# Performance work log

Measured on AMD Instinct MI355X. Metric: run time of the kernel, lower is better.

The kernel has to match this reference:

```python
import jax, jax.numpy as jnp
import numpy as np

N_NODES = 10000
N_EDGES = 320000
D = 128      # node/edge feature dim
H = 512      # MLP hidden width


def _mlp(x, W1, b1, W2, b2):
    return jax.nn.relu(x @ W1 + b1) @ W2 + b2


def setup_inputs() -> dict:
    key = jax.random.key(0)
    ks = jax.random.split(key, 8)
    s = lambda fan_in: 1.0 / np.sqrt(fan_in)
    return {
        "x": jax.random.normal(ks[0], (N_NODES, D), jnp.float32),
        "edge_index": jax.random.randint(ks[1], (2, N_EDGES), 0, N_NODES, jnp.int64),
        "edge_attr": jax.random.normal(ks[2], (N_EDGES, D), jnp.float32),
        "We1": jax.random.normal(ks[3], (3 * D, H), jnp.float32) * s(3 * D),
        "be1": jnp.zeros((H,), jnp.float32),
        "We2": jax.random.normal(ks[4], (H, D), jnp.float32) * s(H),
        "be2": jnp.zeros((D,), jnp.float32),
        "Wn1": jax.random.normal(ks[5], (2 * D, H), jnp.float32) * s(2 * D),
        "bn1": jnp.zeros((H,), jnp.float32),
        "Wn2": jax.random.normal(ks[6], (H, D), jnp.float32) * s(H),
        "bn2": jnp.zeros((D,), jnp.float32),
    }


def reference(x, edge_index, edge_attr, We1, be1, We2, be2, Wn1, bn1, Wn2, bn2):
    senders = edge_index[0]
    receivers = edge_index[1]
    # gather -> edge MLP
    edge_inputs = jnp.concatenate([x[senders], x[receivers], edge_attr], axis=-1)  # [E, 3D]
    updated_edge_attr = _mlp(edge_inputs, We1, be1, We2, be2)                      # [E, D]
    # scatter-add into receiving nodes
    aggregated = jax.ops.segment_sum(updated_edge_attr, receivers, num_segments=x.shape[0])  # [N, D]
    # node MLP
    node_inputs = jnp.concatenate([x, aggregated], axis=-1)                        # [N, 2D]
    updated_nodes = _mlp(node_inputs, Wn1, bn1, Wn2, bn2)                          # [N, D]
    return updated_nodes, updated_edge_attr
```

## Files before the change

### kernel.cpp

```cpp
#include <hip/hip_runtime.h>
#include <hip/hip_bf16.h>

#define N_NODES 10000
#define N_EDGES 320000
#define D 128
#define H 512

typedef __bf16 bf16x8 __attribute__((ext_vector_type(8)));
typedef float f32x4 __attribute__((ext_vector_type(4)));
typedef unsigned short u16x8 __attribute__((ext_vector_type(8)));

__device__ __forceinline__ unsigned short f2bf(float f) {
    union { float f; unsigned u; } v; v.f = f;
    unsigned r = v.u + 0x7fffu + ((v.u >> 16) & 1u);
    return (unsigned short)(r >> 16);
}

__global__ void cast_x_kernel(const float* __restrict__ x, unsigned short* __restrict__ xb) {
    int t = blockIdx.x * 256 + threadIdx.x;
    float4 v = reinterpret_cast<const float4*>(x)[t];
    ushort4 o;
    o.x = f2bf(v.x); o.y = f2bf(v.y); o.z = f2bf(v.z); o.w = f2bf(v.w);
    reinterpret_cast<ushort4*>(xb)[t] = o;
}

__global__ void swizzle_w_kernel(const float* __restrict__ W, unsigned short* __restrict__ out,
                                 int K, int Nn) {
    int t = blockIdx.x * 256 + threadIdx.x;
    int total = (K >> 5) * (Nn >> 4) * 64;
    if (t >= total) return;
    int lane = t & 63;
    int tile = t >> 6;
    int ntiles = Nn >> 4;
    int nt = tile % ntiles;
    int kt = tile / ntiles;
    int k0 = kt * 32 + (lane >> 4) * 8;
    int n  = nt * 16 + (lane & 15);
    unsigned short tmp[8];
#pragma unroll
    for (int j = 0; j < 8; ++j) tmp[j] = f2bf(W[(size_t)(k0 + j) * Nn + n]);
    ushort4* dst = reinterpret_cast<ushort4*>(out + (size_t)t * 8);
    dst[0] = *reinterpret_cast<ushort4*>(&tmp[0]);
    dst[1] = *reinterpret_cast<ushort4*>(&tmp[4]);
}

__global__ __launch_bounds__(256) void edge_mlp_kernel(
    const unsigned short* __restrict__ xb,
    const int* __restrict__ eidx,
    const float* __restrict__ edge_attr,
    const unsigned short* __restrict__ We1s,
    const float* __restrict__ be1,
    const unsigned short* __restrict__ We2s,
    const float* __restrict__ be2,
    float* __restrict__ out_edges,
    float* __restrict__ agg)
{
    __shared__ unsigned short sA[64 * 392];
    __shared__ unsigned short sH[64 * 136];

    const int tid = threadIdx.x;
    const int wave = tid >> 6, lane = tid & 63;
    const int e0 = blockIdx.x * 64;
    const int l15 = lane & 15;
    const int q8 = (lane >> 4) * 8;

#pragma unroll
    for (int seg = 0; seg < 2; ++seg) {
        for (int c = tid; c < 1024; c += 256) {
            int row = c >> 4;
            int off = (c & 15) << 3;
            int e = e0 + row;
            int node = eidx[seg * N_EDGES + e];
            *reinterpret_cast<bf16x8*>(&sA[row * 392 + seg * 128 + off]) =
                *reinterpret_cast<const bf16x8*>(&xb[(size_t)node * 128 + off]);
        }
    }
    for (int c = tid; c < 1024; c += 256) {
        int row = c >> 4;
        int off = (c & 15) << 3;
        int e = e0 + row;
        const float4* src = reinterpret_cast<const float4*>(&edge_attr[(size_t)e * 128 + off]);
        float4 v0 = src[0], v1 = src[1];
        u16x8 o;
        o[0] = f2bf(v0.x); o[1] = f2bf(v0.y); o[2] = f2bf(v0.z); o[3] = f2bf(v0.w);
        o[4] = f2bf(v1.x); o[5] = f2bf(v1.y); o[6] = f2bf(v1.z); o[7] = f2bf(v1.w);
        *reinterpret_cast<u16x8*>(&sA[row * 392 + 256 + off]) = o;
    }
    __syncthreads();

    f32x4 acc2[2][4];
#pragma unroll
    for (int nn = 0; nn < 2; ++nn)
#pragma unroll
        for (int mt = 0; mt < 4; ++mt) acc2[nn][mt] = (f32x4){0.f, 0.f, 0.f, 0.f};

#pragma unroll 1
    for (int h = 0; h < 4; ++h) {
        f32x4 acc1[2][4];
#pragma unroll
        for (int nn = 0; nn < 2; ++nn)
#pragma unroll
            for (int mt = 0; mt < 4; ++mt) acc1[nn][mt] = (f32x4){0.f, 0.f, 0.f, 0.f};

#pragma unroll
        for (int kt = 0; kt < 12; ++kt) {
            bf16x8 a[4];
#pragma unroll
            for (int mt = 0; mt < 4; ++mt)
                a[mt] = *reinterpret_cast<const bf16x8*>(&sA[(mt * 16 + l15) * 392 + kt * 32 + q8]);
#pragma unroll
            for (int nn = 0; nn < 2; ++nn) {
                int ntile = h * 8 + wave * 2 + nn;
                bf16x8 b = *reinterpret_cast<const bf16x8*>(
                    &We1s[(((size_t)kt * 32 + ntile) * 64 + lane) * 8]);
#pragma unroll
                for (int mt = 0; mt < 4; ++mt)
                    acc1[nn][mt] = __builtin_amdgcn_mfma_f32_16x16x32_bf16(a[mt], b, acc1[nn][mt], 0, 0, 0);
            }
        }

        __syncthreads();
#pragma unroll
        for (int nn = 0; nn < 2; ++nn) {
            int cc = (wave * 2 + nn) * 16 + l15;
            float bias = be1[h * 128 + cc];
#pragma unroll
            for (int mt = 0; mt < 4; ++mt)
#pragma unroll
                for (int r = 0; r < 4; ++r) {
                    float v = acc1[nn][mt][r] + bias;
                    v = v > 0.f ? v : 0.f;
                    int row = mt * 16 + (lane >> 4) * 4 + r;
                    sH[row * 136 + cc] = f2bf(v);
                }
        }
        __syncthreads();

#pragma unroll
        for (int kt = 0; kt < 4; ++kt) {
            bf16x8 a[4];
#pragma unroll
            for (int mt = 0; mt < 4; ++mt)
                a[mt] = *reinterpret_cast<const bf16x8*>(&sH[(mt * 16 + l15) * 136 + kt * 32 + q8]);
#pragma unroll
            for (int nn = 0; nn < 2; ++nn) {
                int ntile = wave * 2 + nn;
                bf16x8 b = *reinterpret_cast<const bf16x8*>(
                    &We2s[(((size_t)(h * 4 + kt) * 8 + ntile) * 64 + lane) * 8]);
#pragma unroll
                for (int mt = 0; mt < 4; ++mt)
                    acc2[nn][mt] = __builtin_amdgcn_mfma_f32_16x16x32_bf16(a[mt], b, acc2[nn][mt], 0, 0, 0);
            }
        }
    }

#pragma unroll
    for (int nn = 0; nn < 2; ++nn) {
        int cc = (wave * 2 + nn) * 16 + l15;
        float bias = be2[cc];
#pragma unroll
        for (int mt = 0; mt < 4; ++mt)
#pragma unroll
            for (int r = 0; r < 4; ++r) {
                int row = mt * 16 + (lane >> 4) * 4 + r;
                int e = e0 + row;
                float v = acc2[nn][mt][r] + bias;
                out_edges[(size_t)e * 128 + cc] = v;
                int recv = eidx[N_EDGES + e];
                atomicAdd(&agg[(size_t)recv * 128 + cc], v);
            }
    }
}

__global__ __launch_bounds__(256) void node_mlp_kernel(
    const unsigned short* __restrict__ xb,
    const float* __restrict__ agg,
    const unsigned short* __restrict__ Wn1s,
    const float* __restrict__ bn1,
    const unsigned short* __restrict__ Wn2s,
    const float* __restrict__ bn2,
    float* __restrict__ out_nodes)
{
    __shared__ unsigned short sA[64 * 264];
    __shared__ unsigned short sH[64 * 136];

    const int tid = threadIdx.x;
    const int wave = tid >> 6, lane = tid & 63;
    const int n0 = blockIdx.x * 64;
    const int l15 = lane & 15;
    const int q8 = (lane >> 4) * 8;

    for (int c = tid; c < 1024; c += 256) {
        int row = c >> 4;
        int off = (c & 15) << 3;
        int node = n0 + row;
        bf16x8 v = {};
        if (node < N_NODES)
            v = *reinterpret_cast<const bf16x8*>(&xb[(size_t)node * 128 + off]);
        *reinterpret_cast<bf16x8*>(&sA[row * 264 + off]) = v;
    }
    for (int c = tid; c < 1024; c += 256) {
        int row = c >> 4;
        int off = (c & 15) << 3;
        int node = n0 + row;
        u16x8 o = {0, 0, 0, 0, 0, 0, 0, 0};
        if (node < N_NODES) {
            const float4* src = reinterpret_cast<const float4*>(&agg[(size_t)node * 128 + off]);
            float4 v0 = src[0], v1 = src[1];
            o[0] = f2bf(v0.x); o[1] = f2bf(v0.y); o[2] = f2bf(v0.z); o[3] = f2bf(v0.w);
            o[4] = f2bf(v1.x); o[5] = f2bf(v1.y); o[6] = f2bf(v1.z); o[7] = f2bf(v1.w);
        }
        *reinterpret_cast<u16x8*>(&sA[row * 264 + 128 + off]) = o;
    }
    __syncthreads();

    f32x4 acc2[2][4];
#pragma unroll
    for (int nn = 0; nn < 2; ++nn)
#pragma unroll
        for (int mt = 0; mt < 4; ++mt) acc2[nn][mt] = (f32x4){0.f, 0.f, 0.f, 0.f};

#pragma unroll 1
    for (int h = 0; h < 4; ++h) {
        f32x4 acc1[2][4];
#pragma unroll
        for (int nn = 0; nn < 2; ++nn)
#pragma unroll
            for (int mt = 0; mt < 4; ++mt) acc1[nn][mt] = (f32x4){0.f, 0.f, 0.f, 0.f};

#pragma unroll
        for (int kt = 0; kt < 8; ++kt) {
            bf16x8 a[4];
#pragma unroll
            for (int mt = 0; mt < 4; ++mt)
                a[mt] = *reinterpret_cast<const bf16x8*>(&sA[(mt * 16 + l15) * 264 + kt * 32 + q8]);
#pragma unroll
            for (int nn = 0; nn < 2; ++nn) {
                int ntile = h * 8 + wave * 2 + nn;
                bf16x8 b = *reinterpret_cast<const bf16x8*>(
                    &Wn1s[(((size_t)kt * 32 + ntile) * 64 + lane) * 8]);
#pragma unroll
                for (int mt = 0; mt < 4; ++mt)
                    acc1[nn][mt] = __builtin_amdgcn_mfma_f32_16x16x32_bf16(a[mt], b, acc1[nn][mt], 0, 0, 0);
            }
        }

        __syncthreads();
#pragma unroll
        for (int nn = 0; nn < 2; ++nn) {
            int cc = (wave * 2 + nn) * 16 + l15;
            float bias = bn1[h * 128 + cc];
#pragma unroll
            for (int mt = 0; mt < 4; ++mt)
#pragma unroll
                for (int r = 0; r < 4; ++r) {
                    float v = acc1[nn][mt][r] + bias;
                    v = v > 0.f ? v : 0.f;
                    int row = mt * 16 + (lane >> 4) * 4 + r;
                    sH[row * 136 + cc] = f2bf(v);
                }
        }
        __syncthreads();

#pragma unroll
        for (int kt = 0; kt < 4; ++kt) {
            bf16x8 a[4];
#pragma unroll
            for (int mt = 0; mt < 4; ++mt)
                a[mt] = *reinterpret_cast<const bf16x8*>(&sH[(mt * 16 + l15) * 136 + kt * 32 + q8]);
#pragma unroll
            for (int nn = 0; nn < 2; ++nn) {
                int ntile = wave * 2 + nn;
                bf16x8 b = *reinterpret_cast<const bf16x8*>(
                    &Wn2s[(((size_t)(h * 4 + kt) * 8 + ntile) * 64 + lane) * 8]);
#pragma unroll
                for (int mt = 0; mt < 4; ++mt)
                    acc2[nn][mt] = __builtin_amdgcn_mfma_f32_16x16x32_bf16(a[mt], b, acc2[nn][mt], 0, 0, 0);
            }
        }
    }

#pragma unroll
    for (int nn = 0; nn < 2; ++nn) {
        int cc = (wave * 2 + nn) * 16 + l15;
        float bias = bn2[cc];
#pragma unroll
        for (int mt = 0; mt < 4; ++mt)
#pragma unroll
            for (int r = 0; r < 4; ++r) {
                int row = mt * 16 + (lane >> 4) * 4 + r;
                int node = n0 + row;
                if (node < N_NODES)
                    out_nodes[(size_t)node * 128 + cc] = acc2[nn][mt][r] + bias;
            }
    }
}

extern "C" void kernel_launch(void* const* d_in, const int* in_sizes, int n_in,
                              void* d_out, int out_size, void* d_ws, size_t ws_size,
                              hipStream_t stream) {
    const float* x         = (const float*)d_in[0];
    const int*   eidx      = (const int*)d_in[1];
    const float* edge_attr = (const float*)d_in[2];
    const float* We1       = (const float*)d_in[3];
    const float* be1       = (const float*)d_in[4];
    const float* We2       = (const float*)d_in[5];
    const float* be2       = (const float*)d_in[6];
    const float* Wn1       = (const float*)d_in[7];
    const float* bn1       = (const float*)d_in[8];
    const float* Wn2       = (const float*)d_in[9];
    const float* bn2       = (const float*)d_in[10];
    float* out = (float*)d_out;

    char* ws = (char*)d_ws;
    size_t off = 0;
    auto alloc = [&](size_t bytes) {
        void* p = ws + off;
        off += (bytes + 255) & ~(size_t)255;
        return p;
    };
    unsigned short* xb   = (unsigned short*)alloc((size_t)N_NODES * D * 2);
    unsigned short* We1s = (unsigned short*)alloc((size_t)384 * 512 * 2);
    unsigned short* We2s = (unsigned short*)alloc((size_t)512 * 128 * 2);
    unsigned short* Wn1s = (unsigned short*)alloc((size_t)256 * 512 * 2);
    unsigned short* Wn2s = (unsigned short*)alloc((size_t)512 * 128 * 2);
    float*          agg  = (float*)alloc((size_t)N_NODES * D * 4);

    hipMemsetAsync(agg, 0, (size_t)N_NODES * D * sizeof(float), stream);
    cast_x_kernel<<<(N_NODES * D / 4 + 255) / 256, 256, 0, stream>>>(x, xb);
    swizzle_w_kernel<<<(12 * 32 * 64 + 255) / 256, 256, 0, stream>>>(We1, We1s, 384, 512);
    swizzle_w_kernel<<<(16 * 8 * 64 + 255) / 256, 256, 0, stream>>>(We2, We2s, 512, 128);
    swizzle_w_kernel<<<(8 * 32 * 64 + 255) / 256, 256, 0, stream>>>(Wn1, Wn1s, 256, 512);
    swizzle_w_kernel<<<(16 * 8 * 64 + 255) / 256, 256, 0, stream>>>(Wn2, Wn2s, 512, 128);

    edge_mlp_kernel<<<N_EDGES / 64, 256, 0, stream>>>(
        xb, eidx, edge_attr, We1s, be1, We2s, be2, out + (size_t)N_NODES * D, agg);
    node_mlp_kernel<<<(N_NODES + 63) / 64, 256, 0, stream>>>(
        xb, agg, Wn1s, bn1, Wn2s, bn2, out);
}
```

Baseline: 725.8 us.

## Replace atomic scatter-add with CSR gather aggregation and restructure first-layer GEMM loop

```diff
diff --git a/kernel.cpp b/kernel.cpp
--- a/kernel.cpp
+++ b/kernel.cpp
@@ -44,7 +44,59 @@
     dst[1] = *reinterpret_cast<ushort4*>(&tmp[4]);
 }
 
-__global__ __launch_bounds__(256) void edge_mlp_kernel(
+__global__ void hist_kernel(const int* __restrict__ eidx, int* __restrict__ deg) {
+    int e = blockIdx.x * 256 + threadIdx.x;
+    if (e < N_EDGES) atomicAdd(&deg[eidx[N_EDGES + e]], 1);
+}
+
+__global__ __launch_bounds__(1024) void scan_kernel(const int* __restrict__ deg,
+                                                    int* __restrict__ rowstart,
+                                                    int* __restrict__ cursor) {
+    __shared__ int wsums[16];
+    const int t = threadIdx.x;
+    const int lane = t & 63, wv = t >> 6;
+    const int base = t * 10;
+    int loc[10];
+    int s = 0;
+#pragma unroll
+    for (int i = 0; i < 10; ++i) {
+        int v = (base + i < N_NODES) ? deg[base + i] : 0;
+        loc[i] = s; s += v;
+    }
+    const int tot = s;
+    int inc = tot;
+#pragma unroll
+    for (int d = 1; d < 64; d <<= 1) {
+        int n = __shfl_up(inc, d, 64);
+        if (lane >= d) inc += n;
+    }
+    if (lane == 63) wsums[wv] = inc;
+    __syncthreads();
+    if (t == 0) {
+        int run = 0;
+#pragma unroll
+        for (int w = 0; w < 16; ++w) { int v = wsums[w]; wsums[w] = run; run += v; }
+    }
+    __syncthreads();
+    const int off = wsums[wv] + inc - tot;
+#pragma unroll
+    for (int i = 0; i < 10; ++i) {
+        int idx = base + i;
+        if (idx < N_NODES) { int v = off + loc[i]; rowstart[idx] = v; cursor[idx] = v; }
+    }
+    if (t == 1023) rowstart[N_NODES] = off + tot;
+}
+
+__global__ void scatter_kernel(const int* __restrict__ eidx, int* __restrict__ cursor,
+                               int* __restrict__ elist) {
+    int e = blockIdx.x * 256 + threadIdx.x;
+    if (e < N_EDGES) {
+        int p = atomicAdd(&cursor[eidx[N_EDGES + e]], 1);
+        elist[p] = e;
+    }
+}
+
+__global__ __launch_bounds__(256, 2) void edge_mlp_kernel(
     const unsigned short* __restrict__ xb,
     const int* __restrict__ eidx,
     const float* __restrict__ edge_attr,
@@ -52,8 +104,7 @@
     const float* __restrict__ be1,
     const unsigned short* __restrict__ We2s,
     const float* __restrict__ be2,
-    float* __restrict__ out_edges,
-    float* __restrict__ agg)
+    float* __restrict__ out_edges)
 {
     __shared__ unsigned short sA[64 * 392];
     __shared__ unsigned short sH[64 * 136];
@@ -88,37 +139,36 @@
     }
     __syncthreads();
 
+    f32x4 acc1[8][4];
+#pragma unroll
+    for (int j = 0; j < 8; ++j)
+#pragma unroll
+        for (int mt = 0; mt < 4; ++mt) acc1[j][mt] = (f32x4){0.f, 0.f, 0.f, 0.f};
     f32x4 acc2[2][4];
 #pragma unroll
     for (int nn = 0; nn < 2; ++nn)
 #pragma unroll
         for (int mt = 0; mt < 4; ++mt) acc2[nn][mt] = (f32x4){0.f, 0.f, 0.f, 0.f};
 
-#pragma unroll 1
+#pragma unroll 2
+    for (int kt = 0; kt < 12; ++kt) {
+        bf16x8 a[4];
+#pragma unroll
+        for (int mt = 0; mt < 4; ++mt)
+            a[mt] = *reinterpret_cast<const bf16x8*>(&sA[(mt * 16 + l15) * 392 + kt * 32 + q8]);
+#pragma unroll
+        for (int j = 0; j < 8; ++j) {
+            int ntile = (j >> 1) * 8 + wave * 2 + (j & 1);
+            bf16x8 b = *reinterpret_cast<const bf16x8*>(
+                &We1s[(((size_t)kt * 32 + ntile) * 64 + lane) * 8]);
+#pragma unroll
+            for (int mt = 0; mt < 4; ++mt)
+                acc1[j][mt] = __builtin_amdgcn_mfma_f32_16x16x32_bf16(a[mt], b, acc1[j][mt], 0, 0, 0);
+        }
+    }
+
+#pragma unroll
     for (int h = 0; h < 4; ++h) {
-        f32x4 acc1[2][4];
-#pragma unroll
-        for (int nn = 0; nn < 2; ++nn)
-#pragma unroll
-            for (int mt = 0; mt < 4; ++mt) acc1[nn][mt] = (f32x4){0.f, 0.f, 0.f, 0.f};
-
-#pragma unroll
-        for (int kt = 0; kt < 12; ++kt) {
-            bf16x8 a[4];
-#pragma unroll
-            for (int mt = 0; mt < 4; ++mt)
-                a[mt] = *reinterpret_cast<const bf16x8*>(&sA[(mt * 16 + l15) * 392 + kt * 32 + q8]);
-#pragma unroll
-            for (int nn = 0; nn < 2; ++nn) {
-                int ntile = h * 8 + wave * 2 + nn;
-                bf16x8 b = *reinterpret_cast<const bf16x8*>(
-                    &We1s[(((size_t)kt * 32 + ntile) * 64 + lane) * 8]);
-#pragma unroll
-                for (int mt = 0; mt < 4; ++mt)
-                    acc1[nn][mt] = __builtin_amdgcn_mfma_f32_16x16x32_bf16(a[mt], b, acc1[nn][mt], 0, 0, 0);
-            }
-        }
-
         __syncthreads();
 #pragma unroll
         for (int nn = 0; nn < 2; ++nn) {
@@ -128,7 +178,7 @@
             for (int mt = 0; mt < 4; ++mt)
 #pragma unroll
                 for (int r = 0; r < 4; ++r) {
-                    float v = acc1[nn][mt][r] + bias;
+                    float v = acc1[h * 2 + nn][mt][r] + bias;
                     v = v > 0.f ? v : 0.f;
                     int row = mt * 16 + (lane >> 4) * 4 + r;
                     sH[row * 136 + cc] = f2bf(v);
@@ -163,18 +213,16 @@
 #pragma unroll
             for (int r = 0; r < 4; ++r) {
                 int row = mt * 16 + (lane >> 4) * 4 + r;
-                int e = e0 + row;
-                float v = acc2[nn][mt][r] + bias;
-                out_edges[(size_t)e * 128 + cc] = v;
-                int recv = eidx[N_EDGES + e];
-                atomicAdd(&agg[(size_t)recv * 128 + cc], v);
+                out_edges[(size_t)(e0 + row) * 128 + cc] = acc2[nn][mt][r] + bias;
             }
     }
 }
 
-__global__ __launch_bounds__(256) void node_mlp_kernel(
+__global__ __launch_bounds__(256, 2) void node_mlp_kernel(
     const unsigned short* __restrict__ xb,
-    const float* __restrict__ agg,
+    const float* __restrict__ out_edges,
+    const int* __restrict__ rowstart,
+    const int* __restrict__ elist,
     const unsigned short* __restrict__ Wn1s,
     const float* __restrict__ bn1,
     const unsigned short* __restrict__ Wn2s,
@@ -199,52 +247,65 @@
             v = *reinterpret_cast<const bf16x8*>(&xb[(size_t)node * 128 + off]);
         *reinterpret_cast<bf16x8*>(&sA[row * 264 + off]) = v;
     }
-    for (int c = tid; c < 1024; c += 256) {
-        int row = c >> 4;
-        int off = (c & 15) << 3;
+
+    {
+        int row = tid >> 2, chunk = tid & 3;
         int node = n0 + row;
-        u16x8 o = {0, 0, 0, 0, 0, 0, 0, 0};
+        f32x4 ag[8];
+#pragma unroll
+        for (int q = 0; q < 8; ++q) ag[q] = (f32x4){0.f, 0.f, 0.f, 0.f};
         if (node < N_NODES) {
-            const float4* src = reinterpret_cast<const float4*>(&agg[(size_t)node * 128 + off]);
-            float4 v0 = src[0], v1 = src[1];
-            o[0] = f2bf(v0.x); o[1] = f2bf(v0.y); o[2] = f2bf(v0.z); o[3] = f2bf(v0.w);
-            o[4] = f2bf(v1.x); o[5] = f2bf(v1.y); o[6] = f2bf(v1.z); o[7] = f2bf(v1.w);
-        }
-        *reinterpret_cast<u16x8*>(&sA[row * 264 + 128 + off]) = o;
+            int r0 = rowstart[node], r1 = rowstart[node + 1];
+            for (int j = r0; j < r1; ++j) {
+                int e = elist[j];
+                const f32x4* src =
+                    reinterpret_cast<const f32x4*>(&out_edges[(size_t)e * 128 + chunk * 32]);
+#pragma unroll
+                for (int q = 0; q < 8; ++q) ag[q] += src[q];
+            }
+        }
+#pragma unroll
+        for (int q = 0; q < 4; ++q) {
+            u16x8 o;
+            o[0] = f2bf(ag[2 * q][0]); o[1] = f2bf(ag[2 * q][1]);
+            o[2] = f2bf(ag[2 * q][2]); o[3] = f2bf(ag[2 * q][3]);
+            o[4] = f2bf(ag[2 * q + 1][0]); o[5] = f2bf(ag[2 * q + 1][1]);
+            o[6] = f2bf(ag[2 * q + 1][2]); o[7] = f2bf(ag[2 * q + 1][3]);
+            *reinterpret_cast<u16x8*>(&sA[row * 264 + 128 + chunk * 32 + q * 8]) = o;
+        }
     }
     __syncthreads();
 
+    f32x4 acc1[8][4];
+#pragma unroll
+    for (int j = 0; j < 8; ++j)
+#pragma unroll
+        for (int mt = 0; mt < 4; ++mt) acc1[j][mt] = (f32x4){0.f, 0.f, 0.f, 0.f};
     f32x4 acc2[2][4];
 #pragma unroll
     for (int nn = 0; nn < 2; ++nn)
 #pragma unroll
         for (int mt = 0; mt < 4; ++mt) acc2[nn][mt] = (f32x4){0.f, 0.f, 0.f, 0.f};
 
-#pragma unroll 1
+#pragma unroll 2
+    for (int kt = 0; kt < 8; ++kt) {
+        bf16x8 a[4];
+#pragma unroll
+        for (int mt = 0; mt < 4; ++mt)
+            a[mt] = *reinterpret_cast<const bf16x8*>(&sA[(mt * 16 + l15) * 264 + kt * 32 + q8]);
+#pragma unroll
+        for (int j = 0; j < 8; ++j) {
+            int ntile = (j >> 1) * 8 + wave * 2 + (j & 1);
+            bf16x8 b = *reinterpret_cast<const bf16x8*>(
+                &Wn1s[(((size_t)kt * 32 + ntile) * 64 + lane) * 8]);
+#pragma unroll
+            for (int mt = 0; mt < 4; ++mt)
+                acc1[j][mt] = __builtin_amdgcn_mfma_f32_16x16x32_bf16(a[mt], b, acc1[j][mt], 0, 0, 0);
+        }
+    }
+
+#pragma unroll
     for (int h = 0; h < 4; ++h) {
-        f32x4 acc1[2][4];
-#pragma unroll
-        for (int nn = 0; nn < 2; ++nn)
-#pragma unroll
-            for (int mt = 0; mt < 4; ++mt) acc1[nn][mt] = (f32x4){0.f, 0.f, 0.f, 0.f};
-
-#pragma unroll
-        for (int kt = 0; kt < 8; ++kt) {
-            bf16x8 a[4];
-#pragma unroll
-            for (int mt = 0; mt < 4; ++mt)
-                a[mt] = *reinterpret_cast<const bf16x8*>(&sA[(mt * 16 + l15) * 264 + kt * 32 + q8]);
-#pragma unroll
-            for (int nn = 0; nn < 2; ++nn) {
-                int ntile = h * 8 + wave * 2 + nn;
-                bf16x8 b = *reinterpret_cast<const bf16x8*>(
-                    &Wn1s[(((size_t)kt * 32 + ntile) * 64 + lane) * 8]);
-#pragma unroll
-                for (int mt = 0; mt < 4; ++mt)
-                    acc1[nn][mt] = __builtin_amdgcn_mfma_f32_16x16x32_bf16(a[mt], b, acc1[nn][mt], 0, 0, 0);
-            }
-        }
-
         __syncthreads();
 #pragma unroll
         for (int nn = 0; nn < 2; ++nn) {
@@ -254,7 +315,7 @@
             for (int mt = 0; mt < 4; ++mt)
 #pragma unroll
                 for (int r = 0; r < 4; ++r) {
-                    float v = acc1[nn][mt][r] + bias;
+                    float v = acc1[h * 2 + nn][mt][r] + bias;
                     v = v > 0.f ? v : 0.f;
                     int row = mt * 16 + (lane >> 4) * 4 + r;
                     sH[row * 136 + cc] = f2bf(v);
@@ -324,17 +385,26 @@
     unsigned short* We2s = (unsigned short*)alloc((size_t)512 * 128 * 2);
     unsigned short* Wn1s = (unsigned short*)alloc((size_t)256 * 512 * 2);
     unsigned short* Wn2s = (unsigned short*)alloc((size_t)512 * 128 * 2);
-    float*          agg  = (float*)alloc((size_t)N_NODES * D * 4);
-
-    hipMemsetAsync(agg, 0, (size_t)N_NODES * D * sizeof(float), stream);
+    int* deg      = (int*)alloc((size_t)(N_NODES + 1) * 4);
+    int* rowstart = (int*)alloc((size_t)(N_NODES + 1) * 4);
+    int* cursor   = (int*)alloc((size_t)(N_NODES + 1) * 4);
+    int* elist    = (int*)alloc((size_t)N_EDGES * 4);
+
+    float* out_edges = out + (size_t)N_NODES * D;
+
+    hipMemsetAsync(deg, 0, (size_t)N_NODES * sizeof(int), stream);
     cast_x_kernel<<<(N_NODES * D / 4 + 255) / 256, 256, 0, stream>>>(x, xb);
     swizzle_w_kernel<<<(12 * 32 * 64 + 255) / 256, 256, 0, stream>>>(We1, We1s, 384, 512);
     swizzle_w_kernel<<<(16 * 8 * 64 + 255) / 256, 256, 0, stream>>>(We2, We2s, 512, 128);
     swizzle_w_kernel<<<(8 * 32 * 64 + 255) / 256, 256, 0, stream>>>(Wn1, Wn1s, 256, 512);
     swizzle_w_kernel<<<(16 * 8 * 64 + 255) / 256, 256, 0, stream>>>(Wn2, Wn2s, 512, 128);
 
+    hist_kernel<<<(N_EDGES + 255) / 256, 256, 0, stream>>>(eidx, deg);
+    scan_kernel<<<1, 1024, 0, stream>>>(deg, rowstart, cursor);
+    scatter_kernel<<<(N_EDGES + 255) / 256, 256, 0, stream>>>(eidx, cursor, elist);
+
     edge_mlp_kernel<<<N_EDGES / 64, 256, 0, stream>>>(
-        xb, eidx, edge_attr, We1s, be1, We2s, be2, out + (size_t)N_NODES * D, agg);
+        xb, eidx, edge_attr, We1s, be1, We2s, be2, out_edges);
     node_mlp_kernel<<<(N_NODES + 63) / 64, 256, 0, stream>>>(
-        xb, agg, Wn1s, bn1, Wn2s, bn2, out);
-}
+        xb, out_edges, rowstart, elist, Wn1s, bn1, Wn2s, bn2, out);
+}
```

After: 685.0 us. 5.6% less time.
